# Kernel tuning notes

Hardware: AMD Instinct MI355X
Metric: run time of the kernel (lower is better)

The kernel has to match this reference:

```python
import jax, jax.numpy as jnp
import numpy as np
from jax.scipy.special import logsumexp

B, D, T, O = 8, 64, 512, 256  # batch, channels (d_dim), observed timestamps, grid points


def setup_inputs() -> dict:
    key = jax.random.key(0)
    k1, k2, k3 = jax.random.split(key, 3)
    vals = jax.random.normal(k1, (B, D, T), dtype=jnp.float32)
    mask = (jax.random.uniform(k2, (B, D, T)) < 0.7).astype(jnp.float32)
    mask = mask.at[:, :, 0].set(1.0)  # ensure >=1 observation per (b, channel)
    times = jnp.sort(jax.random.uniform(k3, (B, D, T), dtype=jnp.float32), axis=-1)
    x = jnp.concatenate([vals, mask, times], axis=1)  # (B, 3*D, T)
    grid = jnp.broadcast_to(jnp.linspace(0.0, 1.0, O, dtype=jnp.float32), (B, O))
    kernel = jnp.zeros((D,), dtype=jnp.float32)  # learned per-channel log-bandwidth
    return {"x": x, "interpolation_grid": grid, "kernel": kernel}


def reference(x, interpolation_grid, kernel):
    d_dim = kernel.shape[0]
    x_t = x[:, :d_dim]            # (B, D, T) observed values
    m = x[:, d_dim:2 * d_dim]     # (B, D, T) observation mask in {0,1}
    t = x[:, 2 * d_dim:3 * d_dim] # (B, D, T) observation timestamps

    alpha = jax.nn.softplus(kernel)[None, :, None, None]  # pos_kernel, (1,D,1,1)
    # squared distance between observed times and reference grid: (B,D,T,O)
    norm = (t[:, :, :, None] - interpolation_grid[:, None, None, :]) ** 2
    # log(mask): -inf (clamped) where unobserved, 0 where observed
    logm = jnp.log(jnp.maximum(m, 1e-30))[:, :, :, None]

    s = -alpha * norm + logm                      # (B,D,T,O) masked RBF logits
    w = logsumexp(s, axis=2)                      # (B,D,O) intensity channel
    w1 = jnp.exp(s - w[:, :, None, :])            # softmax over T
    y = jnp.sum(w1 * x_t[:, :, :, None], axis=2)  # (B,D,O) smooth interpolation

    s10 = -10.0 * alpha * norm + logm             # sharper kernel (transient)
    wt_lse = logsumexp(s10, axis=2)
    wt = jnp.exp(s10 - wt_lse[:, :, None, :])
    y_trans = jnp.sum(wt * x_t[:, :, :, None], axis=2)  # (B,D,O)

    return jnp.concatenate([y, w, y_trans], axis=1)  # (B, 3*D, O)
```

## Files before the change

kernel.cpp:

```cpp
#include <hip/hip_runtime.h>
#include <math.h>


namespace {
constexpr int kB = 8, kD = 64, kT = 512, kO = 256;
constexpr int kTH = 512;
constexpr float kLOG2E = 1.4426950408889634f;
constexpr float kLN2   = 0.6931471805599453f;
constexpr float kLM    = 99.65784284662087f;
}

__global__ __launch_bounds__(kTH, 4) void interp_kernel(
    const float* __restrict__ x,
    const float* __restrict__ grid,
    const float* __restrict__ kern,
    float* __restrict__ out)
{
    __shared__ __align__(16) float smem[4096];
    float* s_u = smem;
    float* s_w = smem + kT;
    float* s_v = smem + 2 * kT;

    const int tid  = threadIdx.x;
    const int lane = tid & 63;
    const int wv   = tid >> 6;
    const int ow   = wv & 1;
    const int tq   = wv >> 1;
    const int o0   = ow * 128 + lane;
    const int o1   = o0 + 64;

    const int bd = blockIdx.x;
    const int b  = bd >> 6;
    const int d  = bd & (kD - 1);

    const float* base = x + (size_t)b * (3 * kD * kT);
    const float* Vrow = base + (size_t)d * kT;
    const float* Mrow = base + (size_t)(kD + d) * kT;
    const float* Trow = base + (size_t)(2 * kD + d) * kT;

    const float k     = kern[d];
    const float alpha = fmaxf(k, 0.0f) + log1pf(expf(-fabsf(k)));
    const float a2    = alpha * kLOG2E;

    {
        const float tt = Trow[tid];
        const float mm = Mrow[tid];
        const float lm = fmaf(mm, kLM, -kLM);
        s_u[tid] = fmaf(-a2 * tt, tt, lm);
        s_w[tid] = 2.0f * a2 * tt;
        s_v[tid] = Vrow[tid];
    }
    __syncthreads();

    const float g0 = grid[b * kO + o0];
    const float g1 = grid[b * kO + o1];
    const float c0 = -a2 * g0 * g0;
    const float c1 = -a2 * g1 * g1;

    float l_0=0.f,l_1=0.f, y_0=0.f,y_1=0.f, q_0=0.f,q_1=0.f, z_0=0.f,z_1=0.f;

    const int t0 = tq * 128;
    #pragma unroll 2
    for (int t = t0; t < t0 + 128; t += 4) {
        const float4 uu = *(const float4*)(s_u + t);
        const float4 ww = *(const float4*)(s_w + t);
        const float4 vv = *(const float4*)(s_v + t);

        #pragma unroll
        for (int j = 0; j < 4; ++j) {
            const float u = (&uu.x)[j], w = (&ww.x)[j], v = (&vv.x)[j];
            const float a0 = fmaf(w, g0, u) + c0;
            const float a1 = fmaf(w, g1, u) + c1;
            const float e0 = __builtin_amdgcn_exp2f(a0);
            const float E0 = __builtin_amdgcn_exp2f(10.0f * a0);
            const float e1 = __builtin_amdgcn_exp2f(a1);
            const float E1 = __builtin_amdgcn_exp2f(10.0f * a1);
            l_0 += e0; y_0 = fmaf(e0, v, y_0); q_0 += E0; z_0 = fmaf(E0, v, z_0);
            l_1 += e1; y_1 = fmaf(e1, v, y_1); q_1 += E1; z_1 = fmaf(E1, v, z_1);
        }
    }

    __syncthreads();
    float (*sp)[4][kO] = (float (*)[4][kO])smem;
    sp[tq][0][o0] = l_0;  sp[tq][0][o1] = l_1;
    sp[tq][1][o0] = y_0;  sp[tq][1][o1] = y_1;
    sp[tq][2][o0] = q_0;  sp[tq][2][o1] = q_1;
    sp[tq][3][o0] = z_0;  sp[tq][3][o1] = z_1;
    __syncthreads();

    if (tq == 0) {
        float L0=0.f,L1=0.f, Y0=0.f,Y1=0.f, Q0=0.f,Q1=0.f, Z0=0.f,Z1=0.f;
        #pragma unroll
        for (int j = 0; j < 4; ++j) {
            L0 += sp[j][0][o0]; Y0 += sp[j][1][o0];
            Q0 += sp[j][2][o0]; Z0 += sp[j][3][o0];
            L1 += sp[j][0][o1]; Y1 += sp[j][1][o1];
            Q1 += sp[j][2][o1]; Z1 += sp[j][3][o1];
        }
        const float w0o = __builtin_amdgcn_logf(L0) * kLN2;
        const float w1o = __builtin_amdgcn_logf(L1) * kLN2;
        float* ob = out + (size_t)b * (3 * kD * kO);
        ob[(size_t)d * kO + o0]            = Y0 / L0;
        ob[(size_t)d * kO + o1]            = Y1 / L1;
        ob[(size_t)(kD + d) * kO + o0]     = w0o;
        ob[(size_t)(kD + d) * kO + o1]     = w1o;
        ob[(size_t)(2 * kD + d) * kO + o0] = Z0 / Q0;
        ob[(size_t)(2 * kD + d) * kO + o1] = Z1 / Q1;
    }
}

extern "C" void kernel_launch(void* const* d_in, const int* in_sizes, int n_in,
                              void* d_out, int out_size, void* d_ws, size_t ws_size,
                              hipStream_t stream) {
    const float* x    = (const float*)d_in[0];
    const float* grid = (const float*)d_in[1];
    const float* kern = (const float*)d_in[2];
    float* out        = (float*)d_out;
    interp_kernel<<<dim3(kB * kD), dim3(kTH), 0, stream>>>(x, grid, kern, out);
}
```

Measured before the change: 76.18 us.

## Compact observed timestamps into shared memory and skip masked entries

Each block now uses a wave ballot and prefix count to compact only the observed (mask!=0) timestamps into shared memory, padded to a multiple of 16 with neutral entries. The inner loop then runs over roughly 70% of the timestamps instead of all 512. Masked entries contributed only exp2(-99.66), so dropping them removes exp work that has no numerical effect. The accumulators are also rewritten as float2 pairs in the hope of packed FMA/add codegen. The loop trip count is now data-dependent, so the compile-time unroll is lost, and the prefix step adds an extra barrier.

```diff
diff --git a/kernel.cpp b/kernel.cpp
--- a/kernel.cpp
+++ b/kernel.cpp
@@ -10,16 +10,24 @@
 constexpr float kLM    = 99.65784284662087f;
 }
 
+__device__ __forceinline__ float2 pkfma(float2 a, float b, float2 c) {
+    return make_float2(fmaf(a.x, b, c.x), fmaf(a.y, b, c.y));
+}
+__device__ __forceinline__ float2 pkadd(float2 a, float2 b) {
+    return make_float2(a.x + b.x, a.y + b.y);
+}
+
 __global__ __launch_bounds__(kTH, 4) void interp_kernel(
     const float* __restrict__ x,
     const float* __restrict__ grid,
     const float* __restrict__ kern,
     float* __restrict__ out)
 {
-    __shared__ __align__(16) float smem[4096];
-    float* s_u = smem;
-    float* s_w = smem + kT;
-    float* s_v = smem + 2 * kT;
+    __shared__ __align__(16) float smem[4096 + 8];
+    float* s_u   = smem;
+    float* s_w   = smem + kT;
+    float* s_v   = smem + 2 * kT;
+    float* s_cnt = smem + 4096;
 
     const int tid  = threadIdx.x;
     const int lane = tid & 63;
@@ -42,50 +50,72 @@
     const float alpha = fmaxf(k, 0.0f) + log1pf(expf(-fabsf(k)));
     const float a2    = alpha * kLOG2E;
 
-    {
-        const float tt = Trow[tid];
-        const float mm = Mrow[tid];
-        const float lm = fmaf(mm, kLM, -kLM);
-        s_u[tid] = fmaf(-a2 * tt, tt, lm);
-        s_w[tid] = 2.0f * a2 * tt;
-        s_v[tid] = Vrow[tid];
+    const float tt = Trow[tid];
+    const float mm = Mrow[tid];
+    const float vv = Vrow[tid];
+    const bool keep = (mm != 0.0f);
+    const unsigned long long ball = __ballot(keep);
+    if (lane == 0) s_cnt[wv] = (float)__popcll(ball);
+    __syncthreads();
+
+    int bsum = 0, total = 0;
+    #pragma unroll
+    for (int j = 0; j < 8; ++j) {
+        const int c = (int)s_cnt[j];
+        bsum  += (j < wv) ? c : 0;
+        total += c;
+    }
+    const int padded = (total + 15) & ~15;
+
+    if (keep) {
+        const int pos = bsum + __popcll(ball & ((1ull << lane) - 1ull));
+        s_u[pos] = fmaf(-a2 * tt, tt, 0.0f);
+        s_w[pos] = 2.0f * a2 * tt;
+        s_v[pos] = vv;
+    }
+    if (tid >= total && tid < padded) {
+        s_u[tid] = -500.0f;
+        s_w[tid] = 0.0f;
+        s_v[tid] = 0.0f;
     }
     __syncthreads();
 
     const float g0 = grid[b * kO + o0];
     const float g1 = grid[b * kO + o1];
-    const float c0 = -a2 * g0 * g0;
-    const float c1 = -a2 * g1 * g1;
+    const float2 cc = make_float2(-a2 * g0 * g0, -a2 * g1 * g1);
 
-    float l_0=0.f,l_1=0.f, y_0=0.f,y_1=0.f, q_0=0.f,q_1=0.f, z_0=0.f,z_1=0.f;
+    float2 acc_l = make_float2(0.f, 0.f), acc_y = make_float2(0.f, 0.f);
+    float2 acc_q = make_float2(0.f, 0.f), acc_z = make_float2(0.f, 0.f);
 
-    const int t0 = tq * 128;
-    #pragma unroll 2
-    for (int t = t0; t < t0 + 128; t += 4) {
+    const int chunk = padded >> 2;
+    const int t0 = tq * chunk;
+    for (int t = t0; t < t0 + chunk; t += 4) {
         const float4 uu = *(const float4*)(s_u + t);
         const float4 ww = *(const float4*)(s_w + t);
-        const float4 vv = *(const float4*)(s_v + t);
+        const float4 vs = *(const float4*)(s_v + t);
 
         #pragma unroll
         for (int j = 0; j < 4; ++j) {
-            const float u = (&uu.x)[j], w = (&ww.x)[j], v = (&vv.x)[j];
-            const float a0 = fmaf(w, g0, u) + c0;
-            const float a1 = fmaf(w, g1, u) + c1;
-            const float e0 = __builtin_amdgcn_exp2f(a0);
-            const float E0 = __builtin_amdgcn_exp2f(10.0f * a0);
-            const float e1 = __builtin_amdgcn_exp2f(a1);
-            const float E1 = __builtin_amdgcn_exp2f(10.0f * a1);
-            l_0 += e0; y_0 = fmaf(e0, v, y_0); q_0 += E0; z_0 = fmaf(E0, v, z_0);
-            l_1 += e1; y_1 = fmaf(e1, v, y_1); q_1 += E1; z_1 = fmaf(E1, v, z_1);
+            const float u = (&uu.x)[j], w = (&ww.x)[j], v = (&vs.x)[j];
+            const float2 a = pkadd(pkfma(make_float2(g0, g1), w,
+                                         make_float2(u, u)), cc);
+            const float2 e = make_float2(__builtin_amdgcn_exp2f(a.x),
+                                         __builtin_amdgcn_exp2f(a.y));
+            const float2 E = make_float2(__builtin_amdgcn_exp2f(10.0f * a.x),
+                                         __builtin_amdgcn_exp2f(10.0f * a.y));
+            acc_l = pkadd(acc_l, e);
+            acc_y = pkfma(e, v, acc_y);
+            acc_q = pkadd(acc_q, E);
+            acc_z = pkfma(E, v, acc_z);
         }
     }
 
     __syncthreads();
     float (*sp)[4][kO] = (float (*)[4][kO])smem;
-    sp[tq][0][o0] = l_0;  sp[tq][0][o1] = l_1;
-    sp[tq][1][o0] = y_0;  sp[tq][1][o1] = y_1;
-    sp[tq][2][o0] = q_0;  sp[tq][2][o1] = q_1;
-    sp[tq][3][o0] = z_0;  sp[tq][3][o1] = z_1;
+    sp[tq][0][o0] = acc_l.x;  sp[tq][0][o1] = acc_l.y;
+    sp[tq][1][o0] = acc_y.x;  sp[tq][1][o1] = acc_y.y;
+    sp[tq][2][o0] = acc_q.x;  sp[tq][2][o1] = acc_q.y;
+    sp[tq][3][o0] = acc_z.x;  sp[tq][3][o1] = acc_z.y;
     __syncthreads();
 
     if (tq == 0) {
```

After: 72.48 us. -4.9%, faster.
